# Kernel tuning notes

Measured on AMD Instinct MI355X. Metric: run time of the kernel, lower is better.

The kernel has to match this reference:

```python
import jax, jax.numpy as jnp
import numpy as np

EMB = 1024
HEADS = 16
B, T = 4, 2048


def setup_inputs() -> dict:
    key = jax.random.key(0)
    ks = jax.random.split(key, 9)
    s = 1.0 / np.sqrt(EMB)
    return {
        "x": jax.random.normal(ks[0], (B, T, EMB), dtype=jnp.float32),
        "Wq": jax.random.normal(ks[1], (EMB, EMB), dtype=jnp.float32) * s,
        "bq": jnp.zeros((EMB,), dtype=jnp.float32),
        "Wk": jax.random.normal(ks[2], (EMB, EMB), dtype=jnp.float32) * s,
        "bk": jnp.zeros((EMB,), dtype=jnp.float32),
        "Wv": jax.random.normal(ks[3], (EMB, EMB), dtype=jnp.float32) * s,
        "bv": jnp.zeros((EMB,), dtype=jnp.float32),
        "Wo": jax.random.normal(ks[4], (EMB, EMB), dtype=jnp.float32) * s,
        "bo": jnp.zeros((EMB,), dtype=jnp.float32),
    }


def reference(x, Wq, bq, Wk, bk, Wv, bv, Wo, bo):
    b, t, e = x.shape
    h = HEADS
    hd = e // h
    scale = 1.0 / np.sqrt(hd).astype(np.float32)

    q = (x @ Wq + bq).reshape(b, t, h, hd).transpose(0, 2, 1, 3)  # [b,h,t,hd]
    k = (x @ Wk + bk).reshape(b, t, h, hd).transpose(0, 2, 1, 3)
    v = (x @ Wv + bv).reshape(b, t, h, hd).transpose(0, 2, 1, 3)

    scores = jnp.einsum('bhqd,bhkd->bhqk', q, k) * scale  # [b,h,t,t]
    causal = jnp.tril(jnp.ones((t, t), dtype=bool))  # strict upper triangle masked
    scores = jnp.where(causal, scores, -jnp.inf)
    attn = jax.nn.softmax(scores, axis=-1)
    out = jnp.einsum('bhqk,bhkd->bhqd', attn, v)  # [b,h,t,hd]
    out = out.transpose(0, 2, 1, 3).reshape(b, t, e)
    return out @ Wo + bo
```

## Files before the change

kernel.cpp:

```cpp
#include <hip/hip_runtime.h>
#include <hip/hip_bf16.h>

#define TT   2048
#define NB   4
#define EMB_ 1024
#define NH   16
#define HD   64

typedef __bf16 bf16x8 __attribute__((ext_vector_type(8)));
typedef float  f32x4  __attribute__((ext_vector_type(4)));
typedef short  short4v __attribute__((ext_vector_type(4)));

__device__ inline short f2bf(float f) {
  unsigned u = __builtin_bit_cast(unsigned, f);
  u += 0x7fffu + ((u >> 16) & 1u);
  return (short)(u >> 16);
}

__device__ __forceinline__ unsigned pk2bf(float a, float b) {
  unsigned ua = __builtin_bit_cast(unsigned, a);
  unsigned ub = __builtin_bit_cast(unsigned, b);
  ua += 0x7fffu + ((ua >> 16) & 1u);
  ub += 0x7fffu + ((ub >> 16) & 1u);
  return __builtin_amdgcn_perm(ub, ua, 0x07060302u);
}

__device__ __forceinline__ void gl_lds16(const short* g, short* l) {
  __builtin_amdgcn_global_load_lds(
      (const __attribute__((address_space(1))) unsigned int*)g,
      (__attribute__((address_space(3))) unsigned int*)l, 16, 0, 0);
}

__global__ void convert_w(const float* __restrict__ Wq, const float* __restrict__ Wk,
                          const float* __restrict__ Wv, const float* __restrict__ Wo,
                          short* __restrict__ Wt) {
  __shared__ short tile[32][33];
  const float* W = (blockIdx.z == 0) ? Wq : (blockIdx.z == 1) ? Wk
                   : (blockIdx.z == 2) ? Wv : Wo;
  short* out = Wt + (size_t)blockIdx.z * EMB_ * EMB_;
  int k0 = blockIdx.x * 32, n0 = blockIdx.y * 32;
  int t = threadIdx.x;
  int r = t >> 3, c4 = (t & 7) * 4;
  f32x4 v = *(const f32x4*)&W[(size_t)(k0 + r) * EMB_ + n0 + c4];
#pragma unroll
  for (int j = 0; j < 4; j++) tile[r][c4 + j] = f2bf(v[j]);
  __syncthreads();
  short4v w;
#pragma unroll
  for (int j = 0; j < 4; j++) w[j] = tile[c4 + j][r];
  *(short4v*)&out[(size_t)(n0 + r) * EMB_ + k0 + c4] = w;
}

__global__ void convert_x(const float* __restrict__ x, short* __restrict__ xb) {
  size_t i = ((size_t)blockIdx.x * 256 + threadIdx.x) * 8;
  f32x4 a = *(const f32x4*)&x[i];
  f32x4 b = *(const f32x4*)&x[i + 4];
  short t[8];
#pragma unroll
  for (int j = 0; j < 4; j++) { t[j] = f2bf(a[j]); t[4 + j] = f2bf(b[j]); }
  *(bf16x8*)&xb[i] = *(const bf16x8*)t;
}

__global__ __launch_bounds__(256, 4)
void gemm_lds(const short* __restrict__ A, const short* __restrict__ WtBase,
              const float* __restrict__ b0, const float* __restrict__ b1,
              const float* __restrict__ b2,
              void* O0, void* O1, void* O2, int vmode_z, int o32, int scale_z) {
  __shared__ __align__(16) short As[128 * 64];
  __shared__ __align__(16) short Bs[128 * 64];
  const int tid = threadIdx.x;
  const int z = blockIdx.z;
  const short* W    = WtBase + (size_t)z * EMB_ * EMB_;
  const float* bias = (z == 0) ? b0 : (z == 1) ? b1 : b2;
  void* Out         = (z == 0) ? O0 : (z == 1) ? O1 : O2;
  const bool vmode = (z == vmode_z);
  const float osc = (z == scale_z) ? 0.125f : 1.0f;

  const int m0 = blockIdx.x * 128;
  const int n0 = blockIdx.y * 128;
  const int wave = tid >> 6, lane = tid & 63;
  const int wm = (wave >> 1) * 64, wn = (wave & 1) * 64;
  const int lg = lane >> 4, lc = lane & 15;
  const int srow = lane >> 3, scol = (lane & 7) * 8;

  f32x4 acc[4][4];
#pragma unroll
  for (int i = 0; i < 4; i++)
#pragma unroll
    for (int j = 0; j < 4; j++) acc[i][j] = (f32x4)0.0f;

  for (int kk = 0; kk < EMB_; kk += 64) {
    __syncthreads();
#pragma unroll
    for (int j = 0; j < 4; j++) {
      int rbase = wave * 32 + j * 8;
      gl_lds16(&A[(size_t)(m0 + rbase + srow) * EMB_ + kk + scol], &As[rbase * 64]);
      gl_lds16(&W[(size_t)(n0 + rbase + srow) * EMB_ + kk + scol], &Bs[rbase * 64]);
    }
    __syncthreads();
#pragma unroll
    for (int ks = 0; ks < 2; ks++) {
      bf16x8 af[4], bfr[4];
#pragma unroll
      for (int mi = 0; mi < 4; mi++)
        af[mi] = *(const bf16x8*)&As[(wm + mi * 16 + lc) * 64 + ks * 32 + lg * 8];
#pragma unroll
      for (int ni = 0; ni < 4; ni++)
        bfr[ni] = *(const bf16x8*)&Bs[(wn + ni * 16 + lc) * 64 + ks * 32 + lg * 8];
#pragma unroll
      for (int mi = 0; mi < 4; mi++)
#pragma unroll
        for (int ni = 0; ni < 4; ni++)
          acc[mi][ni] = __builtin_amdgcn_mfma_f32_16x16x32_bf16(af[mi], bfr[ni], acc[mi][ni], 0, 0, 0);
    }
  }

#pragma unroll
  for (int ni = 0; ni < 4; ni++) {
    int col = n0 + wn + ni * 16 + lc;
    float bv = bias[col];
#pragma unroll
    for (int mi = 0; mi < 4; mi++) {
#pragma unroll
      for (int r = 0; r < 4; r++) {
        int row = m0 + wm + mi * 16 + lg * 4 + r;
        float v = (acc[mi][ni][r] + bv) * osc;
        if (vmode) {
          int b = row >> 11, t = row & (TT - 1);
          int h = col >> 6, d = col & (HD - 1);
          ((short*)Out)[((size_t)((b * NH + h) * HD + d)) * TT + t] = f2bf(v);
        } else if (o32) {
          ((float*)Out)[(size_t)row * EMB_ + col] = v;
        } else {
          ((short*)Out)[(size_t)row * EMB_ + col] = f2bf(v);
        }
      }
    }
  }
}

__global__ __launch_bounds__(256, 4)
void gemm_bt(const void* __restrict__ A, int a32,
             const short* __restrict__ WtBase,
             const float* __restrict__ b0, const float* __restrict__ b1,
             const float* __restrict__ b2,
             void* O0, void* O1, void* O2, int vmode_z, int o32, int scale_z) {
  __shared__ __align__(16) short As[128 * 72];
  __shared__ __align__(16) short Bs[128 * 72];
  const int tid = threadIdx.x;
  const int z = blockIdx.z;
  const short* W    = WtBase + (size_t)z * EMB_ * EMB_;
  const float* bias = (z == 0) ? b0 : (z == 1) ? b1 : b2;
  void* Out         = (z == 0) ? O0 : (z == 1) ? O1 : O2;
  const bool vmode = (z == vmode_z);
  const float osc = (z == scale_z) ? 0.125f : 1.0f;

  const int m0 = blockIdx.x * 128;
  const int n0 = blockIdx.y * 128;
  const int wave = tid >> 6, lane = tid & 63;
  const int wm = (wave >> 1) * 64, wn = (wave & 1) * 64;
  const int lg = lane >> 4, lc = lane & 15;

  f32x4 acc[4][4];
#pragma unroll
  for (int i = 0; i < 4; i++)
#pragma unroll
    for (int j = 0; j < 4; j++) acc[i][j] = (f32x4)0.0f;

  for (int kk = 0; kk < EMB_; kk += 64) {
    __syncthreads();
#pragma unroll
    for (int i = 0; i < 4; i++) {
      int s = i * 256 + tid;
      int row = s >> 3, c = s & 7;
      size_t base = (size_t)(m0 + row) * EMB_ + kk + c * 8;
      bf16x8 av;
      if (a32) {
        const float* Af = (const float*)A + base;
        f32x4 u0 = *(const f32x4*)Af;
        f32x4 u1 = *(const f32x4*)(Af + 4);
        short tmp[8];
#pragma unroll
        for (int j = 0; j < 4; j++) { tmp[j] = f2bf(u0[j]); tmp[4 + j] = f2bf(u1[j]); }
        av = *(const bf16x8*)tmp;
      } else {
        av = *(const bf16x8*)((const short*)A + base);
      }
      *(bf16x8*)&As[row * 72 + c * 8] = av;
    }
#pragma unroll
    for (int i = 0; i < 4; i++) {
      int s = i * 256 + tid;
      int row = s >> 3, c = s & 7;
      *(bf16x8*)&Bs[row * 72 + c * 8] =
          *(const bf16x8*)&W[(size_t)(n0 + row) * EMB_ + kk + c * 8];
    }
    __syncthreads();
#pragma unroll
    for (int ks = 0; ks < 2; ks++) {
      bf16x8 af[4], bfr[4];
#pragma unroll
      for (int mi = 0; mi < 4; mi++)
        af[mi] = *(const bf16x8*)&As[(wm + mi * 16 + lc) * 72 + ks * 32 + lg * 8];
#pragma unroll
      for (int ni = 0; ni < 4; ni++)
        bfr[ni] = *(const bf16x8*)&Bs[(wn + ni * 16 + lc) * 72 + ks * 32 + lg * 8];
#pragma unroll
      for (int mi = 0; mi < 4; mi++)
#pragma unroll
        for (int ni = 0; ni < 4; ni++)
          acc[mi][ni] = __builtin_amdgcn_mfma_f32_16x16x32_bf16(af[mi], bfr[ni], acc[mi][ni], 0, 0, 0);
    }
  }

#pragma unroll
  for (int ni = 0; ni < 4; ni++) {
    int col = n0 + wn + ni * 16 + lc;
    float bv = bias[col];
#pragma unroll
    for (int mi = 0; mi < 4; mi++) {
#pragma unroll
      for (int r = 0; r < 4; r++) {
        int row = m0 + wm + mi * 16 + lg * 4 + r;
        float v = (acc[mi][ni][r] + bv) * osc;
        if (vmode) {
          int b = row >> 11, t = row & (TT - 1);
          int h = col >> 6, d = col & (HD - 1);
          ((short*)Out)[((size_t)((b * NH + h) * HD + d)) * TT + t] = f2bf(v);
        } else if (o32) {
          ((float*)Out)[(size_t)row * EMB_ + col] = v;
        } else {
          ((short*)Out)[(size_t)row * EMB_ + col] = f2bf(v);
        }
      }
    }
  }
}

__global__ __launch_bounds__(256, 2)
void attn_fwd(const short* Q, const short* K, const short* Vt, short* O) {
  __shared__ __align__(16) short Ks[128 * 72];
  __shared__ __align__(16) short Vs[64 * 136];
  __shared__ __align__(16) short Ps[4][16 * 72];
  const int tid = threadIdx.x;
  const int bh = blockIdx.y;
  const int b = bh >> 4, h = bh & (NH - 1);
  const int qtA = 15 - (int)blockIdx.x;
  const int qtB = (int)blockIdx.x;
  const int wave = tid >> 6, lane = tid & 63;
  const int lg = lane >> 4, lc = lane & 15;

  bf16x8 qf[2][2][2];
#pragma unroll
  for (int pt = 0; pt < 2; pt++) {
    const int qt = pt ? qtB : qtA;
#pragma unroll
    for (int rb = 0; rb < 2; rb++) {
      const int qrow = b * TT + qt * 128 + rb * 64 + wave * 16 + lc;
      qf[pt][rb][0] = *(const bf16x8*)&Q[(size_t)qrow * EMB_ + h * HD + lg * 8];
      qf[pt][rb][1] = *(const bf16x8*)&Q[(size_t)qrow * EMB_ + h * HD + 32 + lg * 8];
    }
  }

  f32x4 o[2][2][4];
#pragma unroll
  for (int pt = 0; pt < 2; pt++)
#pragma unroll
    for (int rb = 0; rb < 2; rb++)
#pragma unroll
      for (int ni = 0; ni < 4; ni++) o[pt][rb][ni] = (f32x4)0.0f;
  float lsum[2][2] = {{0.f, 0.f}, {0.f, 0.f}};

  bf16x8 kreg[4], vreg[4];

  auto issue_loads = [&](int ktt) {
    const int kb = ktt * 128;
#pragma unroll
    for (int i = 0; i < 4; i++) {
      int s = i * 256 + tid;
      kreg[i] = *(const bf16x8*)&K[(size_t)(b * TT + kb + (s >> 3)) * EMB_ + h * HD + (s & 7) * 8];
      vreg[i] = *(const bf16x8*)&Vt[(size_t)(bh * HD + (s >> 4)) * TT + kb + (s & 15) * 8];
    }
  };
  auto write_lds = [&]() {
#pragma unroll
    for (int i = 0; i < 4; i++) {
      int s = i * 256 + tid;
      *(bf16x8*)&Ks[(s >> 3) * 72 + (s & 7) * 8] = kreg[i];
      *(bf16x8*)&Vs[(s >> 4) * 136 + (s & 15) * 8] = vreg[i];
    }
  };

  auto compute_tile = [&](int qt, bf16x8 (&qft)[2][2], f32x4 (&ot)[2][4],
                          float (&ls)[2], int ktt) {
    const int q0 = qt * 128;
#pragma unroll
    for (int chunk = 0; chunk < 2; chunk++) {
      const int cg = 2 * ktt + chunk;
#pragma unroll
      for (int rb = 0; rb < 2; rb++) {
        const int qbase = q0 + rb * 64 + wave * 16;
        if (cg * 64 > qbase + 15) continue;
        const bool diag = (cg == 2 * qt + rb);
        const int qg = qbase + lc;

        f32x4 s4[4];
#pragma unroll
        for (int ni = 0; ni < 4; ni++) s4[ni] = (f32x4)0.0f;
#pragma unroll
        for (int ks = 0; ks < 2; ks++) {
          bf16x8 kf[4];
#pragma unroll
          for (int ni = 0; ni < 4; ni++)
            kf[ni] = *(const bf16x8*)&Ks[(chunk * 64 + ni * 16 + lc) * 72 + ks * 32 + lg * 8];
#pragma unroll
          for (int ni = 0; ni < 4; ni++)
            s4[ni] = __builtin_amdgcn_mfma_f32_16x16x32_bf16(kf[ni], qft[rb][ks], s4[ni], 0, 0, 0);
        }

#pragma unroll
        for (int ni = 0; ni < 4; ni++) {
          float p[4];
#pragma unroll
          for (int r = 0; r < 4; r++) {
            float v = s4[ni][r];
            if (diag) {
              int keyg = cg * 64 + ni * 16 + lg * 4 + r;
              if (keyg > qg) v = -1e30f;
            }
            p[r] = __expf(v - 6.0f);
            ls[rb] += p[r];
          }
          uint2 dd;
          dd.x = pk2bf(p[0], p[1]);
          dd.y = pk2bf(p[2], p[3]);
          *(uint2*)&Ps[wave][lc * 72 + ni * 16 + lg * 4] = dd;
        }

#pragma unroll
        for (int ks2 = 0; ks2 < 2; ks2++) {
          bf16x8 pa = *(const bf16x8*)&Ps[wave][lc * 72 + ks2 * 32 + lg * 8];
          bf16x8 vf[4];
#pragma unroll
          for (int ni = 0; ni < 4; ni++)
            vf[ni] = *(const bf16x8*)&Vs[(ni * 16 + lc) * 136 + chunk * 64 + ks2 * 32 + lg * 8];
#pragma unroll
          for (int ni = 0; ni < 4; ni++)
            ot[rb][ni] = __builtin_amdgcn_mfma_f32_16x16x32_bf16(pa, vf[ni], ot[rb][ni], 0, 0, 0);
        }
      }
    }
  };

  const int ntiles = qtA + 1;

  issue_loads(0);
  for (int ktt = 0; ktt < ntiles; ktt++) {
    __syncthreads();
    write_lds();
    if (ktt + 1 < ntiles) issue_loads(ktt + 1);
    __syncthreads();

    compute_tile(qtA, qf[0], o[0], lsum[0], ktt);
    if (ktt <= qtB)
      compute_tile(qtB, qf[1], o[1], lsum[1], ktt);
  }

#pragma unroll
  for (int pt = 0; pt < 2; pt++) {
    const int qt = pt ? qtB : qtA;
    const int q0 = qt * 128;
    float linv[2][4];
#pragma unroll
    for (int rb = 0; rb < 2; rb++) {
      float red = lsum[pt][rb];
      red += __shfl_xor(red, 16, 64);
      red += __shfl_xor(red, 32, 64);
#pragma unroll
      for (int r = 0; r < 4; r++)
        linv[rb][r] = 1.0f / __shfl(red, lg * 4 + r, 64);
    }
#pragma unroll
    for (int rb = 0; rb < 2; rb++) {
#pragma unroll
      for (int ni = 0; ni < 4; ni++) {
#pragma unroll
        for (int r = 0; r < 4; r++) {
          int token = b * TT + q0 + rb * 64 + wave * 16 + lg * 4 + r;
          int col = h * HD + ni * 16 + lc;
          O[(size_t)token * EMB_ + col] = f2bf(o[pt][rb][ni][r] * linv[rb][r]);
        }
      }
    }
  }
}

extern "C" void kernel_launch(void* const* d_in, const int* in_sizes, int n_in,
                              void* d_out, int out_size, void* d_ws, size_t ws_size,
                              hipStream_t stream) {
  const float* x  = (const float*)d_in[0];
  const float* Wq = (const float*)d_in[1];
  const float* bq = (const float*)d_in[2];
  const float* Wk = (const float*)d_in[3];
  const float* bk = (const float*)d_in[4];
  const float* Wv = (const float*)d_in[5];
  const float* bv = (const float*)d_in[6];
  const float* Wo = (const float*)d_in[7];
  const float* bo = (const float*)d_in[8];

  short* Wt = (short*)d_ws;
  short* Qb = Wt + (size_t)4 * EMB_ * EMB_;

  convert_w<<<dim3(32, 32, 4), 256, 0, stream>>>(Wq, Wk, Wv, Wo, Wt);

  if (ws_size >= (size_t)40 * 1024 * 1024) {
    short* xb16 = Qb + (size_t)NB * TT * EMB_;
    short* Kb   = (short*)d_out;
    short* Vtb  = Kb + (size_t)NB * TT * EMB_;
    convert_x<<<dim3(4096), 256, 0, stream>>>(x, xb16);
    gemm_lds<<<dim3(64, 8, 3), 256, 0, stream>>>(
        xb16, Wt, bq, bk, bv, Qb, Kb, Vtb, 2, 0, 0);
    attn_fwd<<<dim3(8, 64), 256, 0, stream>>>(Qb, Kb, Vtb, Qb);
    gemm_lds<<<dim3(64, 8, 1), 256, 0, stream>>>(
        Qb, Wt + (size_t)3 * EMB_ * EMB_, bo, bo, bo,
        d_out, d_out, d_out, -1, 1, -1);
  } else if (ws_size >= (size_t)24 * 1024 * 1024) {
    short* Kb  = (short*)d_out;
    short* Vtb = Kb + (size_t)NB * TT * EMB_;
    gemm_bt<<<dim3(64, 8, 3), 256, 0, stream>>>(
        x, 1, Wt, bq, bk, bv, Qb, Kb, Vtb, 2, 0, 0);
    attn_fwd<<<dim3(8, 64), 256, 0, stream>>>(Qb, Kb, Vtb, Qb);
    gemm_bt<<<dim3(64, 8, 1), 256, 0, stream>>>(
        Qb, 0, Wt + (size_t)3 * EMB_ * EMB_, bo, bo, bo,
        d_out, d_out, d_out, -1, 1, -1);
  } else {
    for (int b = 0; b < NB; b++) {
      const float* xb = x + (size_t)b * TT * EMB_;
      float* outb = (float*)d_out + (size_t)b * TT * EMB_;
      short* Kb  = (short*)outb;
      short* Vtb = Kb + (size_t)TT * EMB_;
      gemm_bt<<<dim3(16, 8, 3), 256, 0, stream>>>(
          xb, 1, Wt, bq, bk, bv, Qb, Kb, Vtb, 2, 0, 0);
      attn_fwd<<<dim3(8, 16), 256, 0, stream>>>(Qb, Kb, Vtb, Qb);
      gemm_bt<<<dim3(16, 8, 1), 256, 0, stream>>>(
          Qb, 0, Wt + (size_t)3 * EMB_ * EMB_, bo, bo, bo,
          outb, outb, outb, -1, 1, -1);
    }
  }
}
```

Baseline: 287.4 us.

## Replace projection GEMM with 256x256 double-buffered, swizzled 8-wave pipelined kernel

```diff
diff --git a/kernel.cpp b/kernel.cpp
--- a/kernel.cpp
+++ b/kernel.cpp
@@ -61,66 +61,161 @@
   *(bf16x8*)&xb[i] = *(const bf16x8*)t;
 }
 
-__global__ __launch_bounds__(256, 4)
-void gemm_lds(const short* __restrict__ A, const short* __restrict__ WtBase,
-              const float* __restrict__ b0, const float* __restrict__ b1,
-              const float* __restrict__ b2,
-              void* O0, void* O1, void* O2, int vmode_z, int o32, int scale_z) {
-  __shared__ __align__(16) short As[128 * 64];
-  __shared__ __align__(16) short Bs[128 * 64];
+__global__ __launch_bounds__(512, 2)
+void gemm8(const short* __restrict__ A, const short* __restrict__ W,
+           const float* __restrict__ b0, const float* __restrict__ b1,
+           const float* __restrict__ b2,
+           void* O0, void* O1, void* O2, int vmode_z, int o32, int scale_z) {
+  __shared__ __align__(16) short S[65536];
   const int tid = threadIdx.x;
-  const int z = blockIdx.z;
-  const short* W    = WtBase + (size_t)z * EMB_ * EMB_;
+  const int wave = tid >> 6, lane = tid & 63;
+  const int lg = lane >> 4, lc = lane & 15;
+  const int wm = (wave >> 2) * 128, wn = (wave & 3) * 64;
+  const int m0 = blockIdx.x * 256;
+  const int n0g = blockIdx.y * 256;
+  const int z = n0g >> 10;
   const float* bias = (z == 0) ? b0 : (z == 1) ? b1 : b2;
-  void* Out         = (z == 0) ? O0 : (z == 1) ? O1 : O2;
+  void* Out = (z == 0) ? O0 : (z == 1) ? O1 : O2;
   const bool vmode = (z == vmode_z);
   const float osc = (z == scale_z) ? 0.125f : 1.0f;
 
-  const int m0 = blockIdx.x * 128;
-  const int n0 = blockIdx.y * 128;
-  const int wave = tid >> 6, lane = tid & 63;
-  const int wm = (wave >> 1) * 64, wn = (wave & 1) * 64;
-  const int lg = lane >> 4, lc = lane & 15;
-  const int srow = lane >> 3, scol = (lane & 7) * 8;
-
-  f32x4 acc[4][4];
-#pragma unroll
-  for (int i = 0; i < 4; i++)
+  const int srow = lane >> 3;
+  const int scol = ((lane & 7) ^ srow) * 8;
+  const int g0 = ((0 * 4 + lg) ^ (lc & 7)) * 8;
+  const int g1 = ((1 * 4 + lg) ^ (lc & 7)) * 8;
+
+  f32x4 acc[8][4];
+#pragma unroll
+  for (int i = 0; i < 8; i++)
 #pragma unroll
     for (int j = 0; j < 4; j++) acc[i][j] = (f32x4)0.0f;
 
-  for (int kk = 0; kk < EMB_; kk += 64) {
-    __syncthreads();
-#pragma unroll
-    for (int j = 0; j < 4; j++) {
-      int rbase = wave * 32 + j * 8;
-      gl_lds16(&A[(size_t)(m0 + rbase + srow) * EMB_ + kk + scol], &As[rbase * 64]);
-      gl_lds16(&W[(size_t)(n0 + rbase + srow) * EMB_ + kk + scol], &Bs[rbase * 64]);
-    }
-    __syncthreads();
-#pragma unroll
-    for (int ks = 0; ks < 2; ks++) {
-      bf16x8 af[4], bfr[4];
-#pragma unroll
-      for (int mi = 0; mi < 4; mi++)
-        af[mi] = *(const bf16x8*)&As[(wm + mi * 16 + lc) * 64 + ks * 32 + lg * 8];
-#pragma unroll
-      for (int ni = 0; ni < 4; ni++)
-        bfr[ni] = *(const bf16x8*)&Bs[(wn + ni * 16 + lc) * 64 + ks * 32 + lg * 8];
-#pragma unroll
-      for (int mi = 0; mi < 4; mi++)
-#pragma unroll
-        for (int ni = 0; ni < 4; ni++)
-          acc[mi][ni] = __builtin_amdgcn_mfma_f32_16x16x32_bf16(af[mi], bfr[ni], acc[mi][ni], 0, 0, 0);
-    }
+  auto stA = [&](int buf, int half, int kt) {
+    const int kk = kt * 64;
+#pragma unroll
+    for (int c = 0; c < 2; c++) {
+      const int rl = half * 128 + c * 64 + wave * 8;
+      gl_lds16(&A[(size_t)(m0 + rl + srow) * EMB_ + kk + scol],
+               S + buf * 16384 + rl * 64);
+    }
+  };
+  auto stB = [&](int buf, int half, int kt) {
+    const int kk = kt * 64;
+#pragma unroll
+    for (int c = 0; c < 2; c++) {
+      const int rl = half * 128 + c * 64 + wave * 8;
+      gl_lds16(&W[(size_t)(n0g + rl + srow) * EMB_ + kk + scol],
+               S + 32768 + buf * 16384 + rl * 64);
+    }
+  };
+
+  stA(0, 0, 0); stA(0, 1, 0); stB(0, 0, 0); stB(0, 1, 0);
+  stA(1, 0, 1); stA(1, 1, 1); stB(1, 0, 1); stB(1, 1, 1);
+  asm volatile("s_waitcnt vmcnt(8)" ::: "memory");
+  __builtin_amdgcn_sched_barrier(0);
+  __builtin_amdgcn_s_barrier();
+
+  const int NT = EMB_ / 64;
+  bf16x8 af[4][2], bN01[2][2], bN23[2][2];
+
+#pragma unroll 1
+  for (int kt = 0; kt < NT; kt++) {
+    const int cur = kt & 1, nxt = cur ^ 1;
+    const short* Ac = S + cur * 16384;
+    const short* Bc = S + 32768 + cur * 16384;
+
+#pragma unroll
+    for (int mi = 0; mi < 4; mi++) {
+      af[mi][0] = *(const bf16x8*)&Ac[(wm + mi * 16 + lc) * 64 + g0];
+      af[mi][1] = *(const bf16x8*)&Ac[(wm + mi * 16 + lc) * 64 + g1];
+    }
+#pragma unroll
+    for (int ni = 0; ni < 2; ni++) {
+      bN01[ni][0] = *(const bf16x8*)&Bc[(wn + ni * 16 + lc) * 64 + g0];
+      bN01[ni][1] = *(const bf16x8*)&Bc[(wn + ni * 16 + lc) * 64 + g1];
+    }
+    if (kt > 0 && kt + 1 < NT) stA(nxt, 0, kt + 1);
+    __builtin_amdgcn_s_barrier();
+    asm volatile("s_waitcnt lgkmcnt(0)" ::: "memory");
+    __builtin_amdgcn_sched_barrier(0);
+    __builtin_amdgcn_s_setprio(1);
+#pragma unroll
+    for (int mi = 0; mi < 4; mi++)
+#pragma unroll
+      for (int ni = 0; ni < 2; ni++) {
+        acc[mi][ni] = __builtin_amdgcn_mfma_f32_16x16x32_bf16(af[mi][0], bN01[ni][0], acc[mi][ni], 0, 0, 0);
+        acc[mi][ni] = __builtin_amdgcn_mfma_f32_16x16x32_bf16(af[mi][1], bN01[ni][1], acc[mi][ni], 0, 0, 0);
+      }
+    __builtin_amdgcn_s_setprio(0);
+    __builtin_amdgcn_s_barrier();
+
+#pragma unroll
+    for (int ni = 0; ni < 2; ni++) {
+      bN23[ni][0] = *(const bf16x8*)&Bc[(wn + (ni + 2) * 16 + lc) * 64 + g0];
+      bN23[ni][1] = *(const bf16x8*)&Bc[(wn + (ni + 2) * 16 + lc) * 64 + g1];
+    }
+    if (kt > 0 && kt + 1 < NT) stA(nxt, 1, kt + 1);
+    __builtin_amdgcn_s_barrier();
+    asm volatile("s_waitcnt lgkmcnt(0)" ::: "memory");
+    __builtin_amdgcn_sched_barrier(0);
+    __builtin_amdgcn_s_setprio(1);
+#pragma unroll
+    for (int mi = 0; mi < 4; mi++)
+#pragma unroll
+      for (int ni = 0; ni < 2; ni++) {
+        acc[mi][ni + 2] = __builtin_amdgcn_mfma_f32_16x16x32_bf16(af[mi][0], bN23[ni][0], acc[mi][ni + 2], 0, 0, 0);
+        acc[mi][ni + 2] = __builtin_amdgcn_mfma_f32_16x16x32_bf16(af[mi][1], bN23[ni][1], acc[mi][ni + 2], 0, 0, 0);
+      }
+    __builtin_amdgcn_s_setprio(0);
+    __builtin_amdgcn_s_barrier();
+
+#pragma unroll
+    for (int mi = 0; mi < 4; mi++) {
+      af[mi][0] = *(const bf16x8*)&Ac[(wm + (mi + 4) * 16 + lc) * 64 + g0];
+      af[mi][1] = *(const bf16x8*)&Ac[(wm + (mi + 4) * 16 + lc) * 64 + g1];
+    }
+    if (kt + 2 < NT) stB(cur, 0, kt + 2);
+    __builtin_amdgcn_s_barrier();
+    asm volatile("s_waitcnt lgkmcnt(0)" ::: "memory");
+    __builtin_amdgcn_sched_barrier(0);
+    __builtin_amdgcn_s_setprio(1);
+#pragma unroll
+    for (int mi = 0; mi < 4; mi++)
+#pragma unroll
+      for (int ni = 0; ni < 2; ni++) {
+        acc[mi + 4][ni] = __builtin_amdgcn_mfma_f32_16x16x32_bf16(af[mi][0], bN01[ni][0], acc[mi + 4][ni], 0, 0, 0);
+        acc[mi + 4][ni] = __builtin_amdgcn_mfma_f32_16x16x32_bf16(af[mi][1], bN01[ni][1], acc[mi + 4][ni], 0, 0, 0);
+      }
+    __builtin_amdgcn_s_setprio(0);
+    __builtin_amdgcn_s_barrier();
+
+    if (kt + 2 < NT) stB(cur, 1, kt + 2);
+    __builtin_amdgcn_s_barrier();
+    __builtin_amdgcn_s_setprio(1);
+#pragma unroll
+    for (int mi = 0; mi < 4; mi++)
+#pragma unroll
+      for (int ni = 0; ni < 2; ni++) {
+        acc[mi + 4][ni + 2] = __builtin_amdgcn_mfma_f32_16x16x32_bf16(af[mi][0], bN23[ni][0], acc[mi + 4][ni + 2], 0, 0, 0);
+        acc[mi + 4][ni + 2] = __builtin_amdgcn_mfma_f32_16x16x32_bf16(af[mi][1], bN23[ni][1], acc[mi + 4][ni + 2], 0, 0, 0);
+      }
+    __builtin_amdgcn_s_setprio(0);
+    if (kt == NT - 2) {
+      asm volatile("s_waitcnt vmcnt(0)" ::: "memory");
+    } else if (kt < NT - 2) {
+      asm volatile("s_waitcnt vmcnt(4)" ::: "memory");
+    }
+    __builtin_amdgcn_sched_barrier(0);
+    __builtin_amdgcn_s_barrier();
   }
 
 #pragma unroll
   for (int ni = 0; ni < 4; ni++) {
-    int col = n0 + wn + ni * 16 + lc;
+    int colg = n0g + wn + ni * 16 + lc;
+    int col = colg & (EMB_ - 1);
     float bv = bias[col];
 #pragma unroll
-    for (int mi = 0; mi < 4; mi++) {
+    for (int mi = 0; mi < 8; mi++) {
 #pragma unroll
       for (int r = 0; r < 4; r++) {
         int row = m0 + wm + mi * 16 + lg * 4 + r;
@@ -418,10 +513,10 @@
     short* Kb   = (short*)d_out;
     short* Vtb  = Kb + (size_t)NB * TT * EMB_;
     convert_x<<<dim3(4096), 256, 0, stream>>>(x, xb16);
-    gemm_lds<<<dim3(64, 8, 3), 256, 0, stream>>>(
+    gemm8<<<dim3(32, 12), 512, 0, stream>>>(
         xb16, Wt, bq, bk, bv, Qb, Kb, Vtb, 2, 0, 0);
     attn_fwd<<<dim3(8, 64), 256, 0, stream>>>(Qb, Kb, Vtb, Qb);
-    gemm_lds<<<dim3(64, 8, 1), 256, 0, stream>>>(
+    gemm8<<<dim3(32, 4), 512, 0, stream>>>(
         Qb, Wt + (size_t)3 * EMB_ * EMB_, bo, bo, bo,
         d_out, d_out, d_out, -1, 1, -1);
   } else if (ws_size >= (size_t)24 * 1024 * 1024) {
```

Result: slower. 317.2 us (+10.4%).
